# Kernel tuning notes

Measured on AMD Instinct MI355X. Metric: run time of the kernel, lower is better.

The kernel has to match this reference:

```python
import jax, jax.numpy as jnp
import numpy as np

PHI = (1.0 + 5.0 ** 0.5) / 2.0
B, S, V, D, N, L = 8, 128, 32000, 256, 256, 2


def silu(x):
    return x * jax.nn.sigmoid(x)


def setup_inputs() -> dict:
    key = jax.random.key(0)
    ks = jax.random.split(key, 9)
    inp = {}
    inp["input_ids"] = jax.random.randint(ks[0], (B, S), 0, V)
    # token embedding, init std=0.02 as in _init_weights
    inp["emb"] = 0.02 * jax.random.normal(ks[1], (V, 2 * D), jnp.float32)
    # per-layer resonant params, stacked over layer dim L
    inp["ip_w"] = 0.02 * jax.random.normal(ks[2], (L, D, 2 * D), jnp.float32)  # input_proj weight
    inp["ip_b"] = jnp.zeros((L, D), jnp.float32)                                # input_proj bias
    inp["Wn"] = 0.02 * jax.random.normal(ks[3], (L, N, D), jnp.float32)         # W parameter
    inp["Bn"] = jnp.zeros((L, N, D), jnp.float32)                               # B parameter
    inp["opr"] = 0.02 * jax.random.normal(ks[4], (L, D, N), jnp.float32)        # out_proj_real
    inp["opi"] = 0.02 * jax.random.normal(ks[5], (L, D, N), jnp.float32)        # out_proj_imag
    inp["out_w"] = 0.02 * jax.random.normal(ks[6], (V, 2 * D), jnp.float32)     # output_proj
    inp["out_b"] = jnp.zeros((V,), jnp.float32)
    return inp


def _forward(input_ids, emb, ip_w, ip_b, Wn, Bn, opr, opi, out_w, out_b):
    tok = emb[input_ids]                                  # [B, S, 2D]
    w_emb = jnp.transpose(tok[..., :D], (1, 0, 2))        # [S, B, D] (time-major for scan)
    b_emb = jnp.transpose(tok[..., D:], (1, 0, 2))        # [S, B, D]
    ts = jnp.arange(S, dtype=jnp.float32)                 # t values

    def step(carry, xs):
        h_r, h_i = carry
        w_t, b_t, t = xs
        t_phi = t * PHI
        # Euler transform of recurrent state
        wl = 1.0 + jnp.abs(w_t)                           # [B, D]
        th_r = h_r / wl + b_t + t_phi
        th_i = h_i / wl + b_t + t_phi
        sr, cr = jnp.sin(th_r), jnp.cos(th_r)
        si, ci = jnp.sin(th_i), jnp.cos(th_i)
        h_r_new = cr * ci - sr * si                       # complex rotate
        h_i_new = cr * si + sr * ci
        x_r, x_i = h_r_new, h_i_new
        # resonant layers (residual deltas)
        for l in range(L):
            xc = jnp.concatenate([x_r, x_i], axis=-1) @ ip_w[l].T + ip_b[l]   # [B, D]
            wl_n = 1.0 + jnp.abs(Wn[l])                                        # [N, D]
            theta = xc[:, None, :] / wl_n + Bn[l] + t_phi                      # [B, N, D]
            cos_sum = jnp.cos(theta).sum(-1)                                   # [B, N]
            sin_sum = jnp.sin(theta).sum(-1)                                   # [B, N]
            x_r = x_r + silu(cos_sum @ opr[l].T)
            x_i = x_i + silu(sin_sum @ opi[l].T)
        logits = jnp.concatenate([x_r, x_i], axis=-1) @ out_w.T + out_b       # [B, V]
        return (h_r_new, h_i_new), logits

    h0 = jnp.zeros((B, D), jnp.float32)
    (_, _), logits = jax.lax.scan(step, (h0, h0), (w_emb, b_emb, ts))
    return jnp.transpose(logits, (1, 0, 2))               # [B, S, V]


def reference(input_ids, emb, ip_w, ip_b, Wn, Bn, opr, opi, out_w, out_b):
    return _forward(input_ids, emb, ip_w, ip_b, Wn, Bn, opr, opi, out_w, out_b)
```

## Files before the change

### kernel.cpp

```cpp
#include <hip/hip_runtime.h>
#include <hip/hip_fp16.h>
#include <math.h>


#define PHIF 1.6180339887498949f

typedef unsigned short u16;
typedef __attribute__((ext_vector_type(8))) _Float16 f16x8;
typedef __attribute__((ext_vector_type(4))) float f32x4;

constexpr int B = 8, S = 128, V = 32000, D = 256, N = 256, L = 2;
constexpr int TWO_D = 512;
constexpr int M = S * B;

constexpr size_t OFF_XR   = 0;
constexpr size_t OFF_XI   = OFF_XR   + (size_t)M * D;
constexpr size_t OFF_XC   = OFF_XI   + (size_t)M * D;
constexpr size_t OFF_CS   = OFF_XC   + (size_t)M * D;
constexpr size_t OFF_SS   = OFF_CS   + (size_t)M * N;
constexpr size_t OFF_RWT  = OFF_SS   + (size_t)M * N;
constexpr size_t OFF_BNT  = OFF_RWT  + (size_t)L * N * D;
constexpr size_t OFF_IPWT = OFF_BNT  + (size_t)L * N * D;
constexpr size_t OFF_OPRT = OFF_IPWT + (size_t)L * TWO_D * D;
constexpr size_t OFF_OPIT = OFF_OPRT + (size_t)L * N * D;
constexpr size_t OFF_FLT_END = OFF_OPIT + (size_t)L * N * D;

constexpr size_t A2_BYTE_OFF = OFF_FLT_END * 4;
constexpr size_t W2_BYTE_OFF = A2_BYTE_OFF + (size_t)M * 512 * 2;
constexpr size_t WS_NEED     = W2_BYTE_OFF + (size_t)V * 512 * 2;

__device__ __forceinline__ u16 f2h(float x) {
    return __half_as_ushort(__float2half(x));
}

__global__ void prep_kernel(const float* __restrict__ Wn,
                            const float* __restrict__ Bn,
                            const float* __restrict__ ip_w,
                            const float* __restrict__ opr,
                            const float* __restrict__ opi,
                            float* __restrict__ ws) {
    int i = blockIdx.x * blockDim.x + threadIdx.x;
    if (i < L * N * D) {
        int l = i >> 16;
        int r = i & 65535;
        int a = r >> 8;
        int c = r & 255;
        float wv = Wn[(size_t)l * N * D + (size_t)c * D + a];
        ws[OFF_RWT + i] = 1.0f / (1.0f + fabsf(wv));
        ws[OFF_BNT + i] = Bn[(size_t)l * N * D + (size_t)c * D + a];
        ws[OFF_OPRT + i] = opr[(size_t)l * D * N + (size_t)c * N + a];
        ws[OFF_OPIT + i] = opi[(size_t)l * D * N + (size_t)c * N + a];
    }
    if (i < L * TWO_D * D) {
        int l = i >> 17;
        int r = i & 131071;
        int k = r >> 8;
        int d = r & 255;
        ws[OFF_IPWT + i] = ip_w[(size_t)l * D * TWO_D + (size_t)d * TWO_D + k];
    }
}

__global__ __launch_bounds__(256) void conv_w_kernel(const float* __restrict__ out_w,
                                                     u16* __restrict__ W2) {
    int gid = blockIdx.x * blockDim.x + threadIdx.x;
    if (gid >= V * 128) return;
    int v  = gid >> 7;
    int kq = (gid & 127) << 2;
    float4 x = *(const float4*)&out_w[(size_t)v * TWO_D + kq];
    ushort4 h = {f2h(x.x), f2h(x.y), f2h(x.z), f2h(x.w)};
    *(ushort4*)&W2[(size_t)v * 512 + kq] = h;
}

__global__ __launch_bounds__(256) void conv_a_kernel(const float* __restrict__ ws,
                                                     u16* __restrict__ A2) {
    int gid = blockIdx.x * blockDim.x + threadIdx.x;
    if (gid >= M * 128) return;
    int m  = gid >> 7;
    int kq = (gid & 127) << 2;
    const float* XR = ws + OFF_XR;
    const float* XI = ws + OFF_XI;
    float4 x = (kq < D) ? *(const float4*)&XR[(size_t)m * D + kq]
                        : *(const float4*)&XI[(size_t)m * D + kq - D];
    ushort4 h = {f2h(x.x), f2h(x.y), f2h(x.z), f2h(x.w)};
    *(ushort4*)&A2[(size_t)m * 512 + kq] = h;
}

__global__ __launch_bounds__(64) void recur_kernel(const int* __restrict__ ids,
                                                   const float* __restrict__ emb,
                                                   float* __restrict__ ws) {
    __shared__ int   sid[S];
    __shared__ float swv[S][64];
    __shared__ float sbv[S][64];
    int lane = threadIdx.x;
    int blk  = blockIdx.x;
    int b  = blk >> 2;
    int d  = (blk & 3) * 64 + lane;
    sid[lane]      = ids[b * S + lane];
    sid[64 + lane] = ids[b * S + 64 + lane];
    __syncthreads();
    #pragma unroll 16
    for (int t = 0; t < S; ++t) {
        const float* e = emb + (size_t)sid[t] * TWO_D;
        swv[t][lane] = e[d];
        sbv[t][lane] = e[D + d];
    }
    __syncthreads();
    float* XR = ws + OFF_XR;
    float* XI = ws + OFF_XI;
    float u = 0.f;
    #pragma unroll 8
    for (int t = 0; t < S; ++t) {
        float wl = 1.0f + fabsf(swv[t][lane]);
        float c  = 2.0f * sbv[t][lane] + (2.0f * PHIF) * (float)t;
        float psi = __fdividef(u, wl) + c;
        float sn = __sinf(psi);
        float cs = __cosf(psi);
        size_t row = (size_t)(t * B + b) * D + d;
        XR[row] = cs;
        XI[row] = sn;
        u = cs + sn;
    }
}

__global__ __launch_bounds__(256) void xc_kernel(const float* __restrict__ ipb,
                                                 int l,
                                                 float* __restrict__ ws) {
    __shared__ float xrow[8][TWO_D];
    const float* XR = ws + OFF_XR;
    const float* XI = ws + OFF_XI;
    const float* WT = ws + OFF_IPWT + (size_t)l * TWO_D * D;
    float* XC = ws + OFF_XC;
    int m0 = blockIdx.x * 8;
    int tid = threadIdx.x;
    for (int j = 0; j < 16; ++j) {
        int idx = tid + j * 256;
        int r = idx >> 9;
        int k = idx & 511;
        xrow[r][k] = (k < D) ? XR[(m0 + r) * D + k] : XI[(m0 + r) * D + (k - D)];
    }
    __syncthreads();
    int d = tid;
    float bias = ipb[l * D + d];
    float acc[8];
    #pragma unroll
    for (int r = 0; r < 8; ++r) acc[r] = bias;
    for (int k = 0; k < TWO_D; ++k) {
        float wv = WT[k * D + d];
        #pragma unroll
        for (int r = 0; r < 8; ++r) acc[r] = fmaf(xrow[r][k], wv, acc[r]);
    }
    #pragma unroll
    for (int r = 0; r < 8; ++r) XC[(m0 + r) * D + d] = acc[r];
}

__global__ __launch_bounds__(256) void theta_kernel(int l, float* __restrict__ ws) {
    __shared__ float xls[2][D];
    const float* RWT = ws + OFF_RWT + (size_t)l * D * N;
    const float* BNT = ws + OFF_BNT + (size_t)l * D * N;
    const float* XC = ws + OFF_XC;
    float* CS = ws + OFF_CS;
    float* SS = ws + OFF_SS;
    int tb0 = blockIdx.x * 2;
    int n = threadIdx.x;
    xls[0][n] = XC[(size_t)tb0 * D + n];
    xls[1][n] = XC[(size_t)(tb0 + 1) * D + n];
    __syncthreads();
    float tp0 = (float)(tb0 >> 3) * PHIF;
    float tp1 = (float)((tb0 + 1) >> 3) * PHIF;
    float ac0 = 0.f, as0 = 0.f, ac1 = 0.f, as1 = 0.f;
    #pragma unroll 4
    for (int d = 0; d < D; ++d) {
        float rw = RWT[d * N + n];
        float bn = BNT[d * N + n];
        float th0 = fmaf(xls[0][d], rw, bn) + tp0;
        float th1 = fmaf(xls[1][d], rw, bn) + tp1;
        ac0 += __cosf(th0); as0 += __sinf(th0);
        ac1 += __cosf(th1); as1 += __sinf(th1);
    }
    CS[(size_t)tb0 * N + n] = ac0;
    SS[(size_t)tb0 * N + n] = as0;
    CS[(size_t)(tb0 + 1) * N + n] = ac1;
    SS[(size_t)(tb0 + 1) * N + n] = as1;
}

__global__ __launch_bounds__(256) void update_kernel(int l, float* __restrict__ ws) {
    __shared__ float csh[8][N];
    __shared__ float ssh[8][N];
    const float* CS = ws + OFF_CS;
    const float* SS = ws + OFF_SS;
    const float* WR = ws + OFF_OPRT + (size_t)l * N * D;
    const float* WI = ws + OFF_OPIT + (size_t)l * N * D;
    float* XR = ws + OFF_XR;
    float* XI = ws + OFF_XI;
    int m0 = blockIdx.x * 8;
    int tid = threadIdx.x;
    for (int j = 0; j < 8; ++j) {
        int idx = tid + j * 256;
        int r = idx >> 8;
        int n = idx & 255;
        csh[r][n] = CS[(m0 + r) * N + n];
        ssh[r][n] = SS[(m0 + r) * N + n];
    }
    __syncthreads();
    int d = tid;
    float accr[8] = {0,0,0,0,0,0,0,0};
    float acci[8] = {0,0,0,0,0,0,0,0};
    for (int n = 0; n < N; ++n) {
        float wr = WR[n * D + d];
        float wi = WI[n * D + d];
        #pragma unroll
        for (int r = 0; r < 8; ++r) {
            accr[r] = fmaf(csh[r][n], wr, accr[r]);
            acci[r] = fmaf(ssh[r][n], wi, acci[r]);
        }
    }
    #pragma unroll
    for (int r = 0; r < 8; ++r) {
        float vr = accr[r], vi = acci[r];
        float sgr = 1.0f / (1.0f + expf(-vr));
        float sgi = 1.0f / (1.0f + expf(-vi));
        XR[(m0 + r) * D + d] += vr * sgr;
        XI[(m0 + r) * D + d] += vi * sgi;
    }
}

__global__ __launch_bounds__(256) void logits_mfma_kernel(const u16* __restrict__ A2,
                                                          const u16* __restrict__ W2,
                                                          const float* __restrict__ out_b,
                                                          float* __restrict__ out) {
    __shared__ u16 sA[128 * 32];
    __shared__ u16 sW[128 * 32];
    int rb = blockIdx.x & 7;
    int cb = blockIdx.x >> 3;
    int tid = threadIdx.x;
    int w = tid >> 6, l = tid & 63;
    int wr = w >> 1, wc = w & 1;

    f32x4 acc[4][4];
    #pragma unroll
    for (int i = 0; i < 4; ++i)
        #pragma unroll
        for (int j = 0; j < 4; ++j) acc[i][j] = (f32x4){0.f, 0.f, 0.f, 0.f};

    int srow = l >> 2;
    int sko  = (l & 3) * 8;
    int kg = (l >> 4) * 8;
    int rl = l & 15;

    for (int kk = 0; kk < 512; kk += 32) {
        #pragma unroll
        for (int j = 0; j < 2; ++j) {
            int rloc = (w * 2 + j) * 16 + srow;
            const u16* sa = A2 + (size_t)(rb * 128 + rloc) * 512 + kk + sko;
            const u16* sw = W2 + (size_t)(cb * 128 + rloc) * 512 + kk + sko;
            u16* da = &sA[rloc * 32 + sko];
            u16* dw = &sW[rloc * 32 + sko];
            __builtin_amdgcn_global_load_lds((const __attribute__((address_space(1))) void*)sa,
                                             (__attribute__((address_space(3))) void*)da, 16, 0, 0);
            __builtin_amdgcn_global_load_lds((const __attribute__((address_space(1))) void*)sw,
                                             (__attribute__((address_space(3))) void*)dw, 16, 0, 0);
        }
        __syncthreads();
        f16x8 af[4], wf[4];
        #pragma unroll
        for (int f = 0; f < 4; ++f) {
            af[f] = *(const f16x8*)&sA[(wr * 64 + f * 16 + rl) * 32 + kg];
            wf[f] = *(const f16x8*)&sW[(wc * 64 + f * 16 + rl) * 32 + kg];
        }
        #pragma unroll
        for (int fr = 0; fr < 4; ++fr)
            #pragma unroll
            for (int fc = 0; fc < 4; ++fc)
                acc[fr][fc] = __builtin_amdgcn_mfma_f32_16x16x32_f16(
                    af[fr], wf[fc], acc[fr][fc], 0, 0, 0);
        __syncthreads();
    }

    int rq = l >> 4;
    #pragma unroll
    for (int fc = 0; fc < 4; ++fc) {
        int v = cb * 128 + wc * 64 + fc * 16 + rl;
        float bv = out_b[v];
        #pragma unroll
        for (int fr = 0; fr < 4; ++fr) {
            #pragma unroll
            for (int r = 0; r < 4; ++r) {
                int row = rb * 128 + wr * 64 + fr * 16 + rq * 4 + r;
                int t = row >> 3, b = row & 7;
                out[((size_t)(b * S + t)) * V + v] = acc[fr][fc][r] + bv;
            }
        }
    }
}

constexpr int GBM = 256, GBN = 64, GBK = 32;
constexpr int LDA = GBM + 4;
constexpr int LDW = GBN + 4;

__global__ __launch_bounds__(256) void logits_kernel(const float* __restrict__ out_w,
                                                     const float* __restrict__ out_b,
                                                     const float* __restrict__ ws,
                                                     float* __restrict__ out) {
    __shared__ float As[GBK][LDA];
    __shared__ float Wsh[GBK][LDW];
    const float* XR = ws + OFF_XR;
    const float* XI = ws + OFF_XI;
    int cb = blockIdx.x % (V / GBN);
    int rb = blockIdx.x / (V / GBN);
    int tid = threadIdx.x;
    int tx = tid & 7;
    int ty = tid >> 3;
    int m_base = ty * 8;
    int n0 = tx * 8;
    float acc[8][8];
    #pragma unroll
    for (int r = 0; r < 8; ++r)
        #pragma unroll
        for (int c = 0; c < 8; ++c) acc[r][c] = 0.f;

    for (int kc = 0; kc < TWO_D; kc += GBK) {
        #pragma unroll
        for (int j = 0; j < 32; ++j) {
            int idx = tid + j * 256;
            int k = idx & 31;
            int m = idx >> 5;
            int kgl = kc + k;
            int row = rb * GBM + m;
            As[k][m] = (kgl < D) ? XR[row * D + kgl] : XI[row * D + (kgl - D)];
        }
        #pragma unroll
        for (int j = 0; j < 8; ++j) {
            int idx = tid + j * 256;
            int k = idx & 31;
            int n = idx >> 5;
            Wsh[k][n] = out_w[(size_t)(cb * GBN + n) * TWO_D + kc + k];
        }
        __syncthreads();
        #pragma unroll 8
        for (int k = 0; k < GBK; ++k) {
            float4 a0 = *(const float4*)&As[k][m_base];
            float4 a1 = *(const float4*)&As[k][m_base + 4];
            float4 w0 = *(const float4*)&Wsh[k][n0];
            float4 w1 = *(const float4*)&Wsh[k][n0 + 4];
            float am[8] = {a0.x, a0.y, a0.z, a0.w, a1.x, a1.y, a1.z, a1.w};
            float wn[8] = {w0.x, w0.y, w0.z, w0.w, w1.x, w1.y, w1.z, w1.w};
            #pragma unroll
            for (int r = 0; r < 8; ++r)
                #pragma unroll
                for (int c = 0; c < 8; ++c)
                    acc[r][c] = fmaf(am[r], wn[c], acc[r][c]);
        }
        __syncthreads();
    }
    int v0 = cb * GBN + n0;
    float4 ob0 = *(const float4*)&out_b[v0];
    float4 ob1 = *(const float4*)&out_b[v0 + 4];
    float obn[8] = {ob0.x, ob0.y, ob0.z, ob0.w, ob1.x, ob1.y, ob1.z, ob1.w};
    #pragma unroll
    for (int r = 0; r < 8; ++r) {
        int row = rb * GBM + m_base + r;
        int t = row >> 3;
        int b = row & 7;
        float o[8];
        #pragma unroll
        for (int c = 0; c < 8; ++c) o[c] = acc[r][c] + obn[c];
        *(float4*)&out[((size_t)(b * S + t)) * V + v0]     = *(float4*)&o[0];
        *(float4*)&out[((size_t)(b * S + t)) * V + v0 + 4] = *(float4*)&o[4];
    }
}

extern "C" void kernel_launch(void* const* d_in, const int* in_sizes, int n_in,
                              void* d_out, int out_size, void* d_ws, size_t ws_size,
                              hipStream_t stream) {
    const int*   ids   = (const int*)d_in[0];
    const float* emb   = (const float*)d_in[1];
    const float* ip_w  = (const float*)d_in[2];
    const float* ip_b  = (const float*)d_in[3];
    const float* Wn    = (const float*)d_in[4];
    const float* Bn    = (const float*)d_in[5];
    const float* opr   = (const float*)d_in[6];
    const float* opi   = (const float*)d_in[7];
    const float* out_w = (const float*)d_in[8];
    const float* out_b = (const float*)d_in[9];
    float* out = (float*)d_out;
    float* ws  = (float*)d_ws;
    const bool use_mfma = (ws_size >= WS_NEED);
    u16* A2 = (u16*)((char*)d_ws + A2_BYTE_OFF);
    u16* W2 = (u16*)((char*)d_ws + W2_BYTE_OFF);

    hipLaunchKernelGGL(prep_kernel,  dim3(1024), dim3(256), 0, stream, Wn, Bn, ip_w, opr, opi, ws);
    if (use_mfma)
        hipLaunchKernelGGL(conv_w_kernel, dim3(V * 128 / 256), dim3(256), 0, stream, out_w, W2);
    hipLaunchKernelGGL(recur_kernel, dim3(32), dim3(64), 0, stream, ids, emb, ws);
    for (int l = 0; l < L; ++l) {
        hipLaunchKernelGGL(xc_kernel,     dim3(M / 8), dim3(256), 0, stream, ip_b, l, ws);
        hipLaunchKernelGGL(theta_kernel,  dim3(M / 2), dim3(256), 0, stream, l, ws);
        hipLaunchKernelGGL(update_kernel, dim3(M / 8), dim3(256), 0, stream, l, ws);
    }
    if (use_mfma) {
        hipLaunchKernelGGL(conv_a_kernel, dim3(M * 128 / 256), dim3(256), 0, stream, ws, A2);
        hipLaunchKernelGGL(logits_mfma_kernel, dim3((V / 128) * (M / 128)), dim3(256), 0, stream,
                           A2, W2, out_b, out);
    } else {
        hipLaunchKernelGGL(logits_kernel, dim3((V / GBN) * (M / GBM)), dim3(256), 0, stream,
                           out_w, out_b, ws, out);
    }
}
```

Baseline: 495.0 us.

## Fuse per-layer kernels into one block-resident layers kernel and merge prep conversions

Merges the weight-prep and out_w fp16 conversion into one launch. Replaces the six per-layer xc/theta/update launches, plus the separate fp16 activation conversion, with a single kernel. That kernel keeps four rows' state in shared memory across both layers and writes the fp16 A2 buffer directly. This removes launch overhead and global round-trips of XC/CS/SS. In exchange it uses 256 blocks of 4 rows instead of 8-row or 2-row tiles, so each weight load is reused by fewer rows.

```diff
diff --git a/kernel.cpp b/kernel.cpp
--- a/kernel.cpp
+++ b/kernel.cpp
@@ -33,56 +33,42 @@
     return __half_as_ushort(__float2half(x));
 }
 
-__global__ void prep_kernel(const float* __restrict__ Wn,
-                            const float* __restrict__ Bn,
-                            const float* __restrict__ ip_w,
-                            const float* __restrict__ opr,
-                            const float* __restrict__ opi,
-                            float* __restrict__ ws) {
-    int i = blockIdx.x * blockDim.x + threadIdx.x;
-    if (i < L * N * D) {
-        int l = i >> 16;
-        int r = i & 65535;
-        int a = r >> 8;
-        int c = r & 255;
-        float wv = Wn[(size_t)l * N * D + (size_t)c * D + a];
-        ws[OFF_RWT + i] = 1.0f / (1.0f + fabsf(wv));
-        ws[OFF_BNT + i] = Bn[(size_t)l * N * D + (size_t)c * D + a];
-        ws[OFF_OPRT + i] = opr[(size_t)l * D * N + (size_t)c * N + a];
-        ws[OFF_OPIT + i] = opi[(size_t)l * D * N + (size_t)c * N + a];
-    }
-    if (i < L * TWO_D * D) {
+__global__ __launch_bounds__(256) void prepconv_kernel(const float* __restrict__ Wn,
+                                                       const float* __restrict__ Bn,
+                                                       const float* __restrict__ ip_w,
+                                                       const float* __restrict__ opr,
+                                                       const float* __restrict__ opi,
+                                                       const float* __restrict__ out_w,
+                                                       float* __restrict__ ws,
+                                                       u16* __restrict__ W2) {
+    int blk = blockIdx.x;
+    if (blk < 1024) {
+        int i = blk * 256 + threadIdx.x;
+        if (i < L * N * D) {
+            int l = i >> 16;
+            int r = i & 65535;
+            int a = r >> 8;
+            int c = r & 255;
+            float wv = Wn[(size_t)l * N * D + (size_t)c * D + a];
+            ws[OFF_RWT + i] = 1.0f / (1.0f + fabsf(wv));
+            ws[OFF_BNT + i] = Bn[(size_t)l * N * D + (size_t)c * D + a];
+            ws[OFF_OPRT + i] = opr[(size_t)l * D * N + (size_t)c * N + a];
+            ws[OFF_OPIT + i] = opi[(size_t)l * D * N + (size_t)c * N + a];
+        }
         int l = i >> 17;
         int r = i & 131071;
         int k = r >> 8;
         int d = r & 255;
         ws[OFF_IPWT + i] = ip_w[(size_t)l * D * TWO_D + (size_t)d * TWO_D + k];
-    }
-}
-
-__global__ __launch_bounds__(256) void conv_w_kernel(const float* __restrict__ out_w,
-                                                     u16* __restrict__ W2) {
-    int gid = blockIdx.x * blockDim.x + threadIdx.x;
-    if (gid >= V * 128) return;
-    int v  = gid >> 7;
-    int kq = (gid & 127) << 2;
-    float4 x = *(const float4*)&out_w[(size_t)v * TWO_D + kq];
-    ushort4 h = {f2h(x.x), f2h(x.y), f2h(x.z), f2h(x.w)};
-    *(ushort4*)&W2[(size_t)v * 512 + kq] = h;
-}
-
-__global__ __launch_bounds__(256) void conv_a_kernel(const float* __restrict__ ws,
-                                                     u16* __restrict__ A2) {
-    int gid = blockIdx.x * blockDim.x + threadIdx.x;
-    if (gid >= M * 128) return;
-    int m  = gid >> 7;
-    int kq = (gid & 127) << 2;
-    const float* XR = ws + OFF_XR;
-    const float* XI = ws + OFF_XI;
-    float4 x = (kq < D) ? *(const float4*)&XR[(size_t)m * D + kq]
-                        : *(const float4*)&XI[(size_t)m * D + kq - D];
-    ushort4 h = {f2h(x.x), f2h(x.y), f2h(x.z), f2h(x.w)};
-    *(ushort4*)&A2[(size_t)m * 512 + kq] = h;
+    } else {
+        int gid = (blk - 1024) * 256 + threadIdx.x;
+        if (gid >= V * 128) return;
+        int v  = gid >> 7;
+        int kq = (gid & 127) << 2;
+        float4 x = *(const float4*)&out_w[(size_t)v * TWO_D + kq];
+        ushort4 h = {f2h(x.x), f2h(x.y), f2h(x.z), f2h(x.w)};
+        *(ushort4*)&W2[(size_t)v * 512 + kq] = h;
+    }
 }
 
 __global__ __launch_bounds__(64) void recur_kernel(const int* __restrict__ ids,
@@ -122,105 +108,104 @@
     }
 }
 
-__global__ __launch_bounds__(256) void xc_kernel(const float* __restrict__ ipb,
-                                                 int l,
-                                                 float* __restrict__ ws) {
-    __shared__ float xrow[8][TWO_D];
-    const float* XR = ws + OFF_XR;
-    const float* XI = ws + OFF_XI;
-    const float* WT = ws + OFF_IPWT + (size_t)l * TWO_D * D;
-    float* XC = ws + OFF_XC;
-    int m0 = blockIdx.x * 8;
+__global__ __launch_bounds__(256) void layers_kernel(const float* __restrict__ ipb,
+                                                     float* __restrict__ ws,
+                                                     u16* __restrict__ A2,
+                                                     int use_a2) {
+    __shared__ float xr[4][D];
+    __shared__ float xi[4][D];
+    __shared__ float xc[4][D];
+    __shared__ float cs[4][N];
+    __shared__ float ss[4][N];
+    int m0 = blockIdx.x * 4;
     int tid = threadIdx.x;
-    for (int j = 0; j < 16; ++j) {
-        int idx = tid + j * 256;
-        int r = idx >> 9;
-        int k = idx & 511;
-        xrow[r][k] = (k < D) ? XR[(m0 + r) * D + k] : XI[(m0 + r) * D + (k - D)];
+
+    #pragma unroll
+    for (int r = 0; r < 4; ++r) {
+        xr[r][tid] = ws[OFF_XR + (size_t)(m0 + r) * D + tid];
+        xi[r][tid] = ws[OFF_XI + (size_t)(m0 + r) * D + tid];
+    }
+    float tp[4];
+    #pragma unroll
+    for (int r = 0; r < 4; ++r) tp[r] = (float)((m0 + r) >> 3) * PHIF;
+
+    for (int l = 0; l < L; ++l) {
+        __syncthreads();
+        const float* WT = ws + OFF_IPWT + (size_t)l * TWO_D * D;
+        float bias = ipb[l * D + tid];
+        float a[4];
+        #pragma unroll
+        for (int r = 0; r < 4; ++r) a[r] = bias;
+        #pragma unroll 4
+        for (int k = 0; k < D; ++k) {
+            float wv = WT[k * D + tid];
+            #pragma unroll
+            for (int r = 0; r < 4; ++r) a[r] = fmaf(xr[r][k], wv, a[r]);
+        }
+        #pragma unroll 4
+        for (int k = 0; k < D; ++k) {
+            float wv = WT[(k + D) * D + tid];
+            #pragma unroll
+            for (int r = 0; r < 4; ++r) a[r] = fmaf(xi[r][k], wv, a[r]);
+        }
+        #pragma unroll
+        for (int r = 0; r < 4; ++r) xc[r][tid] = a[r];
+        __syncthreads();
+
+        const float* RW = ws + OFF_RWT + (size_t)l * D * N;
+        const float* BN = ws + OFF_BNT + (size_t)l * D * N;
+        float ac[4] = {0.f, 0.f, 0.f, 0.f};
+        float as[4] = {0.f, 0.f, 0.f, 0.f};
+        #pragma unroll 2
+        for (int d = 0; d < D; ++d) {
+            float rw = RW[d * N + tid];
+            float bn = BN[d * N + tid];
+            #pragma unroll
+            for (int r = 0; r < 4; ++r) {
+                float th = fmaf(xc[r][d], rw, bn) + tp[r];
+                ac[r] += __cosf(th);
+                as[r] += __sinf(th);
+            }
+        }
+        #pragma unroll
+        for (int r = 0; r < 4; ++r) { cs[r][tid] = ac[r]; ss[r][tid] = as[r]; }
+        __syncthreads();
+
+        const float* WR = ws + OFF_OPRT + (size_t)l * N * D;
+        const float* WI = ws + OFF_OPIT + (size_t)l * N * D;
+        float ur[4] = {0.f, 0.f, 0.f, 0.f};
+        float ui[4] = {0.f, 0.f, 0.f, 0.f};
+        #pragma unroll 4
+        for (int n = 0; n < N; ++n) {
+            float wr = WR[n * D + tid];
+            float wi = WI[n * D + tid];
+            #pragma unroll
+            for (int r = 0; r < 4; ++r) {
+                ur[r] = fmaf(cs[r][n], wr, ur[r]);
+                ui[r] = fmaf(ss[r][n], wi, ui[r]);
+            }
+        }
+        #pragma unroll
+        for (int r = 0; r < 4; ++r) {
+            float vr = ur[r], vi = ui[r];
+            float sgr = 1.0f / (1.0f + expf(-vr));
+            float sgi = 1.0f / (1.0f + expf(-vi));
+            xr[r][tid] += vr * sgr;
+            xi[r][tid] += vi * sgi;
+        }
     }
     __syncthreads();
-    int d = tid;
-    float bias = ipb[l * D + d];
-    float acc[8];
-    #pragma unroll
-    for (int r = 0; r < 8; ++r) acc[r] = bias;
-    for (int k = 0; k < TWO_D; ++k) {
-        float wv = WT[k * D + d];
-        #pragma unroll
-        for (int r = 0; r < 8; ++r) acc[r] = fmaf(xrow[r][k], wv, acc[r]);
-    }
-    #pragma unroll
-    for (int r = 0; r < 8; ++r) XC[(m0 + r) * D + d] = acc[r];
-}
-
-__global__ __launch_bounds__(256) void theta_kernel(int l, float* __restrict__ ws) {
-    __shared__ float xls[2][D];
-    const float* RWT = ws + OFF_RWT + (size_t)l * D * N;
-    const float* BNT = ws + OFF_BNT + (size_t)l * D * N;
-    const float* XC = ws + OFF_XC;
-    float* CS = ws + OFF_CS;
-    float* SS = ws + OFF_SS;
-    int tb0 = blockIdx.x * 2;
-    int n = threadIdx.x;
-    xls[0][n] = XC[(size_t)tb0 * D + n];
-    xls[1][n] = XC[(size_t)(tb0 + 1) * D + n];
-    __syncthreads();
-    float tp0 = (float)(tb0 >> 3) * PHIF;
-    float tp1 = (float)((tb0 + 1) >> 3) * PHIF;
-    float ac0 = 0.f, as0 = 0.f, ac1 = 0.f, as1 = 0.f;
-    #pragma unroll 4
-    for (int d = 0; d < D; ++d) {
-        float rw = RWT[d * N + n];
-        float bn = BNT[d * N + n];
-        float th0 = fmaf(xls[0][d], rw, bn) + tp0;
-        float th1 = fmaf(xls[1][d], rw, bn) + tp1;
-        ac0 += __cosf(th0); as0 += __sinf(th0);
-        ac1 += __cosf(th1); as1 += __sinf(th1);
-    }
-    CS[(size_t)tb0 * N + n] = ac0;
-    SS[(size_t)tb0 * N + n] = as0;
-    CS[(size_t)(tb0 + 1) * N + n] = ac1;
-    SS[(size_t)(tb0 + 1) * N + n] = as1;
-}
-
-__global__ __launch_bounds__(256) void update_kernel(int l, float* __restrict__ ws) {
-    __shared__ float csh[8][N];
-    __shared__ float ssh[8][N];
-    const float* CS = ws + OFF_CS;
-    const float* SS = ws + OFF_SS;
-    const float* WR = ws + OFF_OPRT + (size_t)l * N * D;
-    const float* WI = ws + OFF_OPIT + (size_t)l * N * D;
-    float* XR = ws + OFF_XR;
-    float* XI = ws + OFF_XI;
-    int m0 = blockIdx.x * 8;
-    int tid = threadIdx.x;
-    for (int j = 0; j < 8; ++j) {
-        int idx = tid + j * 256;
-        int r = idx >> 8;
-        int n = idx & 255;
-        csh[r][n] = CS[(m0 + r) * N + n];
-        ssh[r][n] = SS[(m0 + r) * N + n];
-    }
-    __syncthreads();
-    int d = tid;
-    float accr[8] = {0,0,0,0,0,0,0,0};
-    float acci[8] = {0,0,0,0,0,0,0,0};
-    for (int n = 0; n < N; ++n) {
-        float wr = WR[n * D + d];
-        float wi = WI[n * D + d];
-        #pragma unroll
-        for (int r = 0; r < 8; ++r) {
-            accr[r] = fmaf(csh[r][n], wr, accr[r]);
-            acci[r] = fmaf(ssh[r][n], wi, acci[r]);
-        }
-    }
-    #pragma unroll
-    for (int r = 0; r < 8; ++r) {
-        float vr = accr[r], vi = acci[r];
-        float sgr = 1.0f / (1.0f + expf(-vr));
-        float sgi = 1.0f / (1.0f + expf(-vi));
-        XR[(m0 + r) * D + d] += vr * sgr;
-        XI[(m0 + r) * D + d] += vi * sgi;
+    #pragma unroll
+    for (int r = 0; r < 4; ++r) {
+        ws[OFF_XR + (size_t)(m0 + r) * D + tid] = xr[r][tid];
+        ws[OFF_XI + (size_t)(m0 + r) * D + tid] = xi[r][tid];
+    }
+    if (use_a2) {
+        #pragma unroll
+        for (int r = 0; r < 4; ++r) {
+            A2[(size_t)(m0 + r) * 512 + tid]       = f2h(xr[r][tid]);
+            A2[(size_t)(m0 + r) * 512 + 256 + tid] = f2h(xi[r][tid]);
+        }
     }
 }
 
@@ -388,17 +373,13 @@
     u16* A2 = (u16*)((char*)d_ws + A2_BYTE_OFF);
     u16* W2 = (u16*)((char*)d_ws + W2_BYTE_OFF);
 
-    hipLaunchKernelGGL(prep_kernel,  dim3(1024), dim3(256), 0, stream, Wn, Bn, ip_w, opr, opi, ws);
-    if (use_mfma)
-        hipLaunchKernelGGL(conv_w_kernel, dim3(V * 128 / 256), dim3(256), 0, stream, out_w, W2);
+    int prep_blocks = 1024 + (use_mfma ? (V * 128 / 256) : 0);
+    hipLaunchKernelGGL(prepconv_kernel, dim3(prep_blocks), dim3(256), 0, stream,
+                       Wn, Bn, ip_w, opr, opi, out_w, ws, W2);
     hipLaunchKernelGGL(recur_kernel, dim3(32), dim3(64), 0, stream, ids, emb, ws);
-    for (int l = 0; l < L; ++l) {
-        hipLaunchKernelGGL(xc_kernel,     dim3(M / 8), dim3(256), 0, stream, ip_b, l, ws);
-        hipLaunchKernelGGL(theta_kernel,  dim3(M / 2), dim3(256), 0, stream, l, ws);
-        hipLaunchKernelGGL(update_kernel, dim3(M / 8), dim3(256), 0, stream, l, ws);
-    }
+    hipLaunchKernelGGL(layers_kernel, dim3(M / 4), dim3(256), 0, stream,
+                       ip_b, ws, A2, use_mfma ? 1 : 0);
     if (use_mfma) {
-        hipLaunchKernelGGL(conv_a_kernel, dim3(M * 128 / 256), dim3(256), 0, stream, ws, A2);
         hipLaunchKernelGGL(logits_mfma_kernel, dim3((V / 128) * (M / 128)), dim3(256), 0, stream,
                            A2, W2, out_b, out);
     } else {
```

Measured after the change: 521.4 us. 5.3% more time.
